# Kernel optimization log

Hardware: AMD Instinct MI355X
Metric: run time of the kernel (lower is better)

Reference implementation:

```python
import jax, jax.numpy as jnp
import numpy as np

NH, HD, MBS = 32, 64, 16   # num_heads, head_dim, mini_batch_size
BASE_LR = 1.0
ROPE_BASE = 10000.0
EPS = 1e-6


def _rotate_half(x):
    x1, x2 = jnp.split(x, 2, axis=-1)
    return jnp.concatenate((-x2, x1), axis=-1)


def _permute_qk(x):
    B, H, L, D = x.shape
    return x.reshape(B, H, L, D // 2, 2).swapaxes(-1, -2).reshape(B, H, L, D)


def _undo_permute_qk(x):
    B, H, L, D = x.shape
    return x.reshape(B, H, L, 2, D // 2).swapaxes(-1, -2).reshape(B, H, L, D)


def _ln_fwd(x, gamma, beta):
    mu = x.mean(-1, keepdims=True)
    var = x.var(-1, keepdims=True)
    return gamma * ((x - mu) / jnp.sqrt(var + EPS)) + beta


def _ln_fused_l2_bwd(x, target, gamma, beta):
    # grad of 0.5*||LN(x) - target||^2 wrt x, fused
    D = x.shape[-1]
    mu = x.mean(-1, keepdims=True)
    std = jnp.sqrt(x.var(-1, keepdims=True) + EPS)
    x_hat = (x - mu) / std
    y = gamma * x_hat + beta
    g = (y - target) * gamma
    return (D * g - g.sum(-1, keepdims=True) - x_hat * (g * x_hat).sum(-1, keepdims=True)) / (D * std)


def setup_inputs() -> dict:
    key = jax.random.key(0)
    ks = jax.random.split(key, 8)
    B, L, C, OUT = 4, 2048, 2048, 768
    s = 0.02
    return {
        "hidden_states": jax.random.normal(ks[0], (B, L, C), jnp.float32),
        "position_ids": jnp.broadcast_to(jnp.arange(L, dtype=jnp.int32)[None], (B, L)),
        "Wq": jax.random.normal(ks[1], (C, C), jnp.float32) * s,
        "Wk": jax.random.normal(ks[2], (C, C), jnp.float32) * s,
        "Wv": jax.random.normal(ks[3], (C, C), jnp.float32) * s,
        "Wo": jax.random.normal(ks[4], (C, OUT), jnp.float32) * s,
        "W1": jax.random.normal(ks[5], (NH, HD, HD), jnp.float32) * s,
        "b1": jnp.zeros((NH, 1, HD), jnp.float32),
        "ttt_lr_weight": jax.random.normal(ks[6], (NH, 1, C), jnp.float32) * s,
        "ttt_lr_bias": jnp.zeros((NH, 1), jnp.float32),
        "learnable_token_idx": jnp.zeros((MBS,), jnp.float32),
        "ttt_norm_weight": jnp.ones((NH, HD), jnp.float32),
        "ttt_norm_bias": jnp.zeros((NH, HD), jnp.float32),
        "post_norm_weight": jnp.ones((C,), jnp.float32),
        "post_norm_bias": jnp.zeros((C,), jnp.float32),
    }


def reference(hidden_states, position_ids, Wq, Wk, Wv, Wo, W1, b1,
              ttt_lr_weight, ttt_lr_bias, learnable_token_idx,
              ttt_norm_weight, ttt_norm_bias, post_norm_weight, post_norm_bias):
    B, L, C = hidden_states.shape
    NM = L // MBS
    # QKV projections -> [B, NH, L, HD]
    XQ = (hidden_states @ Wq).reshape(B, L, NH, HD).transpose(0, 2, 1, 3)
    XK = (hidden_states @ Wk).reshape(B, L, NH, HD).transpose(0, 2, 1, 3)
    XV = (hidden_states @ Wv).reshape(B, L, NH, HD).transpose(0, 2, 1, 3)
    # RoPE on positions modulo the mini-batch size
    pos = (position_ids % MBS).astype(jnp.float32)  # [B, L]
    inv_freq = 1.0 / (ROPE_BASE ** (jnp.arange(0, HD, 2, dtype=jnp.float32) / HD))
    freqs = pos[..., None] * inv_freq               # [B, L, HD/2]
    emb = jnp.concatenate((freqs, freqs), axis=-1)  # [B, L, HD]
    cos = jnp.cos(emb)[:, None]                     # [B, 1, L, HD]
    sin = jnp.sin(emb)[:, None]
    XQ, XK = _permute_qk(XQ), _permute_qk(XK)
    XQ = XQ * cos + _rotate_half(XQ) * sin
    XK = XK * cos + _rotate_half(XK) * sin
    XQ, XK = _undo_permute_qk(XQ), _undo_permute_qk(XK)
    # reshape into mini-batches: [B, NH, NM, K, HD]
    X = hidden_states.reshape(B, NM, MBS, C)
    XQ = XQ.reshape(B, NH, NM, MBS, HD)
    XK = XK.reshape(B, NH, NM, MBS, HD)
    XV = XV.reshape(B, NH, NM, MBS, HD)
    # eta: per-token learnable LR gate
    ttt_lr = jax.nn.sigmoid(
        jnp.einsum('bnkc,hdc->bhnkd', X, ttt_lr_weight)
        + ttt_lr_bias.reshape(1, NH, 1, 1, 1))              # [B,NH,NM,K,1]
    ttt_lr_eta = BASE_LR * ttt_lr.transpose(0, 1, 2, 4, 3) / HD  # [B,NH,NM,1,K]
    token_idx = jnp.clip(1.0 / jnp.arange(1, MBS + 1, dtype=jnp.float32)
                         + learnable_token_idx, 0.0, None)
    token_eta = token_idx.reshape(1, 1, 1, MBS, 1)
    eta = token_eta * ttt_lr_eta                            # [B,NH,NM,K,K]
    # TTT-Linear dual-form mini-batch scan
    ln_w = ttt_norm_weight.reshape(1, NH, 1, HD)
    ln_b = ttt_norm_bias.reshape(1, NH, 1, HD)
    W1_0 = jnp.broadcast_to(W1[None], (B, NH, HD, HD))
    b1_0 = jnp.broadcast_to(b1[None], (B, NH, 1, HD))
    tril = jnp.tril(jnp.ones((MBS, MBS), hidden_states.dtype))

    def step(carry, xs):
        W1_s, b1_s = carry
        xq, xk, xv, eta_m = xs                 # [B,NH,K,HD], eta_m [B,NH,K,K]
        Z1 = xk @ W1_s + b1_s
        target = xv - xk
        grad = _ln_fused_l2_bwd(Z1, target, ln_w, ln_b)
        Attn = tril * (xq @ xk.swapaxes(-1, -2))
        b1_bar = b1_s - (tril * eta_m) @ grad
        Z1_bar = xq @ W1_s - (eta_m * Attn) @ grad + b1_bar
        last_eta = eta_m[:, :, -1, :, None]    # [B,NH,K,1]
        W1_new = W1_s - (last_eta * xk).swapaxes(-1, -2) @ grad
        b1_new = b1_s - jnp.sum(last_eta * grad, axis=-2, keepdims=True)
        out = xq + _ln_fwd(Z1_bar, ln_w, ln_b)
        return (W1_new, b1_new), out

    xs = (XQ.transpose(2, 0, 1, 3, 4), XK.transpose(2, 0, 1, 3, 4),
          XV.transpose(2, 0, 1, 3, 4), eta.transpose(2, 0, 1, 3, 4))
    _, outs = jax.lax.scan(step, (W1_0, b1_0), xs)   # [NM,B,NH,K,HD]
    out = outs.transpose(1, 2, 0, 3, 4).reshape(B, NH, L, HD)
    out = out.transpose(0, 2, 1, 3).reshape(B, L, C)
    # post LayerNorm (eps 1e-6) and output projection
    mu = out.mean(-1, keepdims=True)
    var = out.var(-1, keepdims=True)
    out = (out - mu) / jnp.sqrt(var + EPS) * post_norm_weight + post_norm_bias
    return out @ Wo
```

## Files before the change

### kernel.cpp

```cpp
#include <hip/hip_runtime.h>
#include <cstddef>
#include <cstdint>

#define B_DIM   4
#define L_SEQ   2048
#define C_DIM   2048
#define OUT_DIM 768
#define NHEADS  32
#define HDIM    64
#define MBS_    16
#define NMINI   128
#define EPS_    1e-6f

typedef _Float16 half8 __attribute__((ext_vector_type(8)));
typedef _Float16 half4 __attribute__((ext_vector_type(4)));
typedef float floatx4 __attribute__((ext_vector_type(4)));

__device__ __forceinline__ void glds16(const void* g, void* l) {
    __builtin_amdgcn_global_load_lds(
        (const __attribute__((address_space(1))) uint32_t*)g,
        (__attribute__((address_space(3))) uint32_t*)l, 16, 0, 0);
}

__device__ __forceinline__ void split8(const float4 a, const float4 b,
                                       half8& hi, half8& lo) {
    const float x[8] = {a.x, a.y, a.z, a.w, b.x, b.y, b.z, b.w};
#pragma unroll
    for (int e = 0; e < 8; e++) {
        const _Float16 h = (_Float16)x[e];
        hi[e] = h;
        lo[e] = (_Float16)(x[e] - (float)h);
    }
}

__device__ __forceinline__ void split4(const float4 a, half4& hi, half4& lo) {
    const float x[4] = {a.x, a.y, a.z, a.w};
#pragma unroll
    for (int e = 0; e < 4; e++) {
        const _Float16 h = (_Float16)x[e];
        hi[e] = h;
        lo[e] = (_Float16)(x[e] - (float)h);
    }
}

__device__ __forceinline__ uint32_t pack_hl(float v) {
    const _Float16 h = (_Float16)v;
    const _Float16 l = (_Float16)(v - (float)h);
    union { _Float16 f[2]; uint32_t u; } p;
    p.f[0] = h; p.f[1] = l;
    return p.u;
}

__device__ __forceinline__ half8 pairswap(half8 v) {
    union { half8 h; uint32_t u[4]; } a, b;
    a.h = v;
#pragma unroll
    for (int e = 0; e < 4; e++) b.u[e] = (a.u[e] >> 16) | (a.u[e] << 16);
    return b.h;
}

template<int CTRL>
__device__ __forceinline__ float dpp_add(float v) {
    const int x = __builtin_amdgcn_update_dpp(0, __float_as_int(v), CTRL, 0xF, 0xF, false);
    return v + __int_as_float(x);
}
__device__ __forceinline__ float red16(float v) {
    v = dpp_add<0xB1>(v);
    v = dpp_add<0x4E>(v);
    v = dpp_add<0x124>(v);
    v = dpp_add<0x128>(v);
    return v;
}

__device__ __forceinline__ void bar_lgkm() {
    asm volatile("s_waitcnt lgkmcnt(0)\n\ts_barrier" ::: "memory");
}

__global__ __launch_bounds__(256)
void asplit_kernel(const float* __restrict__ A, _Float16* __restrict__ Ahi,
                   _Float16* __restrict__ Alo)
{
    const size_t idx = ((size_t)blockIdx.x * 256 + threadIdx.x) * 16;
    half8 h0, l0, h1, l1;
    {
        const float4 a = *(const float4*)(A + idx);
        const float4 b = *(const float4*)(A + idx + 4);
        split8(a, b, h0, l0);
    }
    {
        const float4 a = *(const float4*)(A + idx + 8);
        const float4 b = *(const float4*)(A + idx + 12);
        split8(a, b, h1, l1);
    }
    *(half8*)(Ahi + idx)     = h0;
    *(half8*)(Ahi + idx + 8) = h1;
    *(half8*)(Alo + idx)     = l0;
    *(half8*)(Alo + idx + 8) = l1;
}

__global__ __launch_bounds__(512)
void gemm8(const _Float16* __restrict__ Ahi, const _Float16* __restrict__ Alo,
           const _Float16* __restrict__ Bhi, const _Float16* __restrict__ Blo,
           float* __restrict__ Cout, int Ndim, int mode, int doRope)
{
    __shared__ __align__(16) _Float16 sAh[3][8192];
    __shared__ __align__(16) _Float16 sAl[3][8192];
    __shared__ __align__(16) _Float16 sBh[3][4096];
    __shared__ __align__(16) _Float16 sBl[3][4096];
    const int tid = threadIdx.x;
    const int nbx = Ndim >> 7;
    const int nwg = gridDim.x;
    int lin = blockIdx.x;
    lin = (lin & 7) * (nwg >> 3) + (lin >> 3);
    const int m0 = (lin / nbx) * 256;
    const int n0 = (lin % nbx) * 128;
    const int K = 2048;

    size_t gA[2];
    int lA[2];
#pragma unroll
    for (int X = 0; X < 2; X++) {
        const int c = X * 512 + tid;
        const int row = c >> 2, s = c & 3;
        const int ks = s ^ ((row >> 1) & 3);
        gA[X] = (size_t)(m0 + row) * K + ks * 8;
        lA[X] = c * 8;
    }
    size_t gB;
    int lB;
    {
        const int row = tid >> 2, s = tid & 3;
        const int ks = s ^ ((row >> 1) & 3);
        gB = (size_t)(n0 + row) * K + ks * 8;
        lB = tid * 8;
    }

    const int lane = tid & 63, q = lane >> 4, lc = lane & 15;
    const int w = tid >> 6, wm = w >> 1, wn = w & 1;
    int offA[4], offB[4];
#pragma unroll
    for (int i = 0; i < 4; i++) {
        const int rA = wm * 64 + i * 16 + lc;
        offA[i] = rA * 32 + ((q ^ ((rA >> 1) & 3)) << 3);
    }
#pragma unroll
    for (int j = 0; j < 4; j++) {
        const int rB = wn * 64 + j * 16 + lc;
        offB[j] = rB * 32 + ((q ^ ((rB >> 1) & 3)) << 3);
    }

    floatx4 acc[4][4];
#pragma unroll
    for (int i = 0; i < 4; i++)
#pragma unroll
        for (int j = 0; j < 4; j++) acc[i][j] = (floatx4)0.0f;

#define STAGE(T)                                                         \
    {                                                                    \
        const int b_ = (T) % 3;                                          \
        const int ko_ = (T) * 32;                                        \
        glds16(Ahi + gA[0] + ko_, &sAh[b_][lA[0]]);                      \
        glds16(Alo + gA[0] + ko_, &sAl[b_][lA[0]]);                      \
        glds16(Ahi + gA[1] + ko_, &sAh[b_][lA[1]]);                      \
        glds16(Alo + gA[1] + ko_, &sAl[b_][lA[1]]);                      \
        glds16(Bhi + gB + ko_,    &sBh[b_][lB]);                         \
        glds16(Blo + gB + ko_,    &sBl[b_][lB]);                         \
    }

#define FRAGS(B_)                                                        \
    half8 ah[4], al[4], bh[4], bl[4];                                    \
    _Pragma("unroll")                                                    \
    for (int i = 0; i < 4; i++) {                                        \
        ah[i] = *(const half8*)&sAh[B_][offA[i]];                        \
        al[i] = *(const half8*)&sAl[B_][offA[i]];                        \
    }                                                                    \
    _Pragma("unroll")                                                    \
    for (int j = 0; j < 4; j++) {                                        \
        bh[j] = *(const half8*)&sBh[B_][offB[j]];                        \
        bl[j] = *(const half8*)&sBl[B_][offB[j]];                        \
    }

#define MFMAS                                                            \
    __builtin_amdgcn_s_setprio(1);                                       \
    _Pragma("unroll")                                                    \
    for (int i = 0; i < 4; i++)                                          \
        _Pragma("unroll")                                                \
        for (int j = 0; j < 4; j++) {                                    \
            acc[i][j] = __builtin_amdgcn_mfma_f32_16x16x32_f16(ah[i], bh[j], acc[i][j], 0, 0, 0); \
            acc[i][j] = __builtin_amdgcn_mfma_f32_16x16x32_f16(ah[i], bl[j], acc[i][j], 0, 0, 0); \
            acc[i][j] = __builtin_amdgcn_mfma_f32_16x16x32_f16(al[i], bh[j], acc[i][j], 0, 0, 0); \
        }                                                                \
    __builtin_amdgcn_s_setprio(0);

    STAGE(0)
    STAGE(1)
    asm volatile("s_waitcnt vmcnt(6) lgkmcnt(0)\n\ts_barrier" ::: "memory");

    for (int t = 0; t < 62; t++) {
        const int b = t % 3;
        FRAGS(b)
        STAGE(t + 2)
        MFMAS
        asm volatile("s_waitcnt vmcnt(6) lgkmcnt(0)\n\ts_barrier" ::: "memory");
    }
    {
        FRAGS(2)
        MFMAS
        asm volatile("s_waitcnt vmcnt(0) lgkmcnt(0)\n\ts_barrier" ::: "memory");
    }
    {
        FRAGS(0)
        MFMAS
    }
#undef STAGE
#undef FRAGS
#undef MFMAS

    float cs[4][4], sn[4][4];
    if (doRope) {
#pragma unroll
        for (int j = 0; j < 4; j++) {
            const int ii = ((j * 16 + lc) & 63) >> 1;
            const float invf = expf(-(float)ii * 0.28782313662425574f);
#pragma unroll
            for (int r = 0; r < 4; r++) {
                const float ang = (float)(q * 4 + r) * invf;
                sincosf(ang, &sn[j][r], &cs[j][r]);
            }
        }
    }
    const int oddcol = lc & 1;
#pragma unroll
    for (int i = 0; i < 4; i++) {
#pragma unroll
        for (int j = 0; j < 4; j++) {
            floatx4 v = acc[i][j];
            if (doRope) {
#pragma unroll
                for (int r = 0; r < 4; r++) {
                    const float partner = __shfl_xor(v[r], 1);
                    v[r] = v[r] * cs[j][r] + partner * (oddcol ? sn[j][r] : -sn[j][r]);
                }
            }
            const int n = n0 + wn * 64 + j * 16 + lc;
            if (mode == 0) {
                const int h = (n >> 6) & 31, d = n & 63;
#pragma unroll
                for (int r = 0; r < 4; r++) {
                    const int m = m0 + wm * 64 + i * 16 + q * 4 + r;
                    const int b = m >> 11, li = m & 2047;
                    Cout[((size_t)(b * 32 + h) * 2048 + li) * 64 + d] = v[r];
                }
            } else {
#pragma unroll
                for (int r = 0; r < 4; r++) {
                    const int m = m0 + wm * 64 + i * 16 + q * 4 + r;
                    Cout[(size_t)m * OUT_DIM + n] = v[r];
                }
            }
        }
    }
}

__global__ __launch_bounds__(256)
void gemm_f32(const float* __restrict__ A,
              const _Float16* __restrict__ Bhi, const _Float16* __restrict__ Blo,
              float* __restrict__ Cout, int mode, int doRope)
{
    __shared__ __align__(16) float    sA[4096];
    __shared__ __align__(16) _Float16 sBhi[4096];
    __shared__ __align__(16) _Float16 sBlo[4096];
    const int tid = threadIdx.x;
    const int m0 = blockIdx.y * 128, n0 = blockIdx.x * 128;
    const int K = 2048;

    size_t gA[4]; float* lA[4];
#pragma unroll
    for (int I = 0; I < 4; I++) {
        const int c = I * 256 + tid;
        const int row = c >> 3, seg = (c & 7) ^ (row & 7);
        gA[I] = (size_t)(m0 + row) * K + seg * 4;
        lA[I] = &sA[c * 4];
    }
    size_t gB[2]; _Float16 *lBh[2], *lBl[2];
#pragma unroll
    for (int I = 0; I < 2; I++) {
        const int c = I * 256 + tid;
        const int row = c >> 2, seg = (c & 3) ^ ((row >> 1) & 3);
        gB[I] = (size_t)(n0 + row) * K + seg * 8;
        lBh[I] = &sBhi[c * 8];
        lBl[I] = &sBlo[c * 8];
    }

    const int lane = tid & 63, quad = lane >> 4, lc = lane & 15;
    const int wv = tid >> 6, wm = wv & 1, wn = wv >> 1;
    int offA0[4], offA1[4], offB[4];
#pragma unroll
    for (int i = 0; i < 4; i++) {
        const int rA = wm * 64 + i * 16 + lc;
        offA0[i] = (rA * 8 + ((2 * quad)     ^ (rA & 7))) * 4;
        offA1[i] = (rA * 8 + ((2 * quad + 1) ^ (rA & 7))) * 4;
    }
#pragma unroll
    for (int j = 0; j < 4; j++) {
        const int rB = wn * 64 + j * 16 + lc;
        offB[j] = (rB * 4 + (quad ^ ((rB >> 1) & 3))) * 8;
    }

    floatx4 acc[4][4];
#pragma unroll
    for (int i = 0; i < 4; i++)
#pragma unroll
        for (int j = 0; j < 4; j++) acc[i][j] = (floatx4)0.0f;

    for (int k0 = 0; k0 < K; k0 += 32) {
        __syncthreads();
#pragma unroll
        for (int I = 0; I < 4; I++) glds16(A + gA[I] + k0, lA[I]);
#pragma unroll
        for (int I = 0; I < 2; I++) {
            glds16(Bhi + gB[I] + k0, lBh[I]);
            glds16(Blo + gB[I] + k0, lBl[I]);
        }
        __syncthreads();

        half8 ah[4], al[4], bh[4], bl[4];
#pragma unroll
        for (int i = 0; i < 4; i++) {
            const float4 va = *(const float4*)&sA[offA0[i]];
            const float4 vb = *(const float4*)&sA[offA1[i]];
            split8(va, vb, ah[i], al[i]);
        }
#pragma unroll
        for (int j = 0; j < 4; j++) {
            bh[j] = *(const half8*)&sBhi[offB[j]];
            bl[j] = *(const half8*)&sBlo[offB[j]];
        }
#pragma unroll
        for (int i = 0; i < 4; i++)
#pragma unroll
            for (int j = 0; j < 4; j++) {
                acc[i][j] = __builtin_amdgcn_mfma_f32_16x16x32_f16(ah[i], bh[j], acc[i][j], 0, 0, 0);
                acc[i][j] = __builtin_amdgcn_mfma_f32_16x16x32_f16(ah[i], bl[j], acc[i][j], 0, 0, 0);
                acc[i][j] = __builtin_amdgcn_mfma_f32_16x16x32_f16(al[i], bh[j], acc[i][j], 0, 0, 0);
            }
    }

    float cs[4][4], sn[4][4];
    if (doRope) {
#pragma unroll
        for (int j = 0; j < 4; j++) {
            const int ii = ((j * 16 + lc) & 63) >> 1;
            const float invf = expf(-(float)ii * 0.28782313662425574f);
#pragma unroll
            for (int r = 0; r < 4; r++) {
                const float ang = (float)(quad * 4 + r) * invf;
                sincosf(ang, &sn[j][r], &cs[j][r]);
            }
        }
    }
    const int oddcol = lc & 1;
#pragma unroll
    for (int i = 0; i < 4; i++) {
#pragma unroll
        for (int j = 0; j < 4; j++) {
            floatx4 v = acc[i][j];
            if (doRope) {
#pragma unroll
                for (int r = 0; r < 4; r++) {
                    const float partner = __shfl_xor(v[r], 1);
                    v[r] = v[r] * cs[j][r] + partner * (oddcol ? sn[j][r] : -sn[j][r]);
                }
            }
            const int n = n0 + wn * 64 + j * 16 + lc;
            if (mode == 0) {
                const int h = (n >> 6) & 31, d = n & 63;
#pragma unroll
                for (int r = 0; r < 4; r++) {
                    const int m = m0 + wm * 64 + i * 16 + quad * 4 + r;
                    const int b = m >> 11, li = m & 2047;
                    Cout[((size_t)(b * 32 + h) * 2048 + li) * 64 + d] = v[r];
                }
            } else {
#pragma unroll
                for (int r = 0; r < 4; r++) {
                    const int m = m0 + wm * 64 + i * 16 + quad * 4 + r;
                    Cout[(size_t)m * OUT_DIM + n] = v[r];
                }
            }
        }
    }
}

__global__ __launch_bounds__(256)
void wtrans_kernel(const float* __restrict__ W, _Float16* __restrict__ BThi,
                   _Float16* __restrict__ BTlo, int Nw)
{
    __shared__ float tile[32][33];
    const int t = threadIdx.x, tx = t & 31, ty = t >> 5;
    const int n0 = blockIdx.x * 32, k0 = blockIdx.y * 32;
    const int K = 2048;
#pragma unroll
    for (int r = 0; r < 4; r++)
        tile[ty + r * 8][tx] = W[(size_t)(k0 + ty + r * 8) * Nw + n0 + tx];
    __syncthreads();
#pragma unroll
    for (int r = 0; r < 4; r++) {
        const float val = tile[tx][ty + r * 8];
        const _Float16 hh = (_Float16)val;
        const size_t o = (size_t)(n0 + ty + r * 8) * K + k0 + tx;
        BThi[o] = hh;
        BTlo[o] = (_Float16)(val - (float)hh);
    }
}

__global__ __launch_bounds__(256)
void lr_kernel(const float* __restrict__ hidden, const float* __restrict__ wlr,
               const float* __restrict__ lr_bias, float* __restrict__ lrs)
{
    __shared__ float sRow[2048];
    __shared__ float sPart[32][9];
    const int m = blockIdx.x;
    const int t = threadIdx.x;
    const float* row = hidden + (size_t)m * C_DIM;
#pragma unroll
    for (int j = 0; j < 8; j++) sRow[t + j * 256] = row[t + j * 256];
    __syncthreads();
    const int h = t >> 3, p = t & 7;
    const float* w = wlr + (size_t)h * C_DIM;
    float s = 0.0f;
#pragma unroll 8
    for (int k = 0; k < 64; k++) {
        const int c = k * 32 + p * 4;
        const float4 a = *(const float4*)(sRow + c);
        const float4 b = *(const float4*)(w + c);
        s += a.x * b.x + a.y * b.y + a.z * b.z + a.w * b.w;
    }
    sPart[h][p] = s;
    __syncthreads();
    if (t < 32) {
        float v = 0.0f;
#pragma unroll
        for (int p2 = 0; p2 < 8; p2++) v += sPart[t][p2];
        v += lr_bias[t];
        const float sig = 1.0f / (1.0f + expf(-v));
        lrs[((size_t)(m >> 11) * NHEADS + t) * L_SEQ + (m & 2047)] = sig;
    }
}

__global__ __launch_bounds__(256, 1)
void scan_mfma(const float* __restrict__ XQ, const float* __restrict__ XK,
               float* __restrict__ XVo, const float* __restrict__ LRS,
               const float* __restrict__ W1i, const float* __restrict__ b1i,
               const float* __restrict__ lt, const float* __restrict__ lnw,
               const float* __restrict__ lnb)
{
    __shared__ __align__(16) _Float16 sXqH[1024], sXqL[1024];
    __shared__ __align__(16) _Float16 sXkH[1024], sXkL[1024];
    __shared__ __align__(16) float    sTgt[16 * 68];
    __shared__ __align__(16) float    sXq32[2][16 * 68];
    __shared__ __align__(16) _Float16 sW1H[4096], sW1L[4096];
    __shared__ __align__(16) uint32_t sKT[64 * 20];
    __shared__ __align__(16) uint32_t sCf[16 * 20];
    __shared__ __align__(16) float sRedA[16 * 36];
    __shared__ __align__(16) float sRedC[16 * 12];
    __shared__ __align__(16) float sEta[16];
    __shared__ float sB1[64];

    const int bh = blockIdx.x, h = bh & 31;
    const int t = threadIdx.x;
    const int lane = t & 63, q = lane >> 4, lc = lane & 15;
    const int w = t >> 6;
    const int col = w * 16 + lc;
    const int iRow = t >> 4;
    const int m = t & 15;

    if (t < 64) sB1[t] = b1i[h * 64 + t];

    float w1s[4][4];
#pragma unroll
    for (int t4 = 0; t4 < 4; t4++)
#pragma unroll
        for (int r = 0; r < 4; r++) {
            const float v = W1i[h * 4096 + (16 * t4 + lc) * 64 + (16 * w + 4 * q + r)];
            w1s[t4][r] = v;
            const int nn = 16 * w + 4 * q + r, k = 16 * t4 + lc;
            const int off = nn * 64 + ((((k >> 3) ^ (nn & 7)) << 3) | (k & 7));
            const _Float16 hh = (_Float16)v;
            sW1H[off] = hh; sW1L[off] = (_Float16)(v - (float)hh);
        }

    const float gamC = lnw[h * 64 + col], betC = lnb[h * 64 + col];
    const float g2c = gamC * gamC;
    float sumG2 = 0.0f;
#pragma unroll
    for (int d0 = 0; d0 < 16; d0++) {
        const float4 gv = *(const float4*)(lnw + h * 64 + d0 * 4);
        sumG2 += gv.x * gv.x + gv.y * gv.y + gv.z * gv.z + gv.w * gv.w;
    }
    float tokR[4];
#pragma unroll
    for (int r = 0; r < 4; r++)
        tokR[r] = fmaxf(1.0f / (float)(4 * q + r + 1) + lt[4 * q + r], 0.0f);
    const float tok15 = fmaxf(1.0f / 16.0f + lt[15], 0.0f);

    __syncthreads();

    const size_t base = (size_t)bh * L_SEQ * HDIM;
    const float* xq_g = XQ + base;
    const float* xk_g = XK + base;
    float* xv_g = XVo + base;
    const float* lr_g = LRS + (size_t)bh * L_SEQ;

    float4 cq = *(const float4*)(xq_g + t * 4);
    float4 ck = *(const float4*)(xk_g + t * 4);
    float4 cv = *(const float4*)(xv_g + t * 4);
    float clr = lr_g[m];

    const int rw = 16 * w + lc;
    const int stOff = iRow * 64 + ((((m >> 1) ^ (iRow & 7)) << 3) | ((m & 1) << 2));
    const int gkm = (m ^ (m >> 2)) & 3;
    const int ktWb = 4 * (w ^ gkm) + q;

    for (int n = 0; n < NMINI; n++) {
        const int buf = n & 1;
        {
            half4 hq, lq, hk, lk;
            split4(cq, hq, lq);
            split4(ck, hk, lk);
            *(half4*)&sXqH[stOff] = hq;
            *(half4*)&sXqL[stOff] = lq;
            *(half4*)&sXkH[stOff] = hk;
            *(half4*)&sXkL[stOff] = lk;
            const float4 tg = make_float4(cv.x - ck.x, cv.y - ck.y,
                                          cv.z - ck.z, cv.w - ck.w);
            *(float4*)&sTgt[iRow * 68 + m * 4] = tg;
            *(float4*)&sXq32[buf][iRow * 68 + m * 4] = cq;
            const float kvv[4] = {ck.x, ck.y, ck.z, ck.w};
#pragma unroll
            for (int i2 = 0; i2 < 4; i2++)
                sKT[(4 * m + i2) * 20 + ktWb] = pack_hl(kvv[i2]);
        }
        if (t < 16) sEta[t] = clr * (1.0f / 64.0f);
        const int np = (n + 1) & (NMINI - 1);
        const float4 nq = *(const float4*)(xq_g + np * 1024 + t * 4);
        const float4 nk = *(const float4*)(xk_g + np * 1024 + t * 4);
        const float4 nv = *(const float4*)(xv_g + np * 1024 + t * 4);
        const float nlr = lr_g[np * 16 + m];
        bar_lgkm();

        const float b1c = sB1[col];
        const float4 ev = *(const float4*)&sEta[4 * q];
        const float evv[4] = {ev.x, ev.y, ev.z, ev.w};

        half8 qh[2], ql[2], kh[2], kl[2], wh[2], wl[2];
#pragma unroll
        for (int f = 0; f < 2; f++) {
            const int cx = ((4 * f + q) ^ (lc & 7)) << 3;
            qh[f] = *(const half8*)&sXqH[lc * 64 + cx];
            ql[f] = *(const half8*)&sXqL[lc * 64 + cx];
            kh[f] = *(const half8*)&sXkH[lc * 64 + cx];
            kl[f] = *(const half8*)&sXkL[lc * 64 + cx];
            const int cw = ((4 * f + q) ^ (rw & 7)) << 3;
            wh[f] = *(const half8*)&sW1H[rw * 64 + cw];
            wl[f] = *(const half8*)&sW1L[rw * 64 + cw];
        }

        floatx4 z1a = (floatx4)0.0f, zba = (floatx4)0.0f, at = (floatx4)0.0f;
#pragma unroll
        for (int f = 0; f < 2; f++) {
            z1a = __builtin_amdgcn_mfma_f32_16x16x32_f16(kh[f], wh[f], z1a, 0, 0, 0);
            z1a = __builtin_amdgcn_mfma_f32_16x16x32_f16(kh[f], wl[f], z1a, 0, 0, 0);
            z1a = __builtin_amdgcn_mfma_f32_16x16x32_f16(kl[f], wh[f], z1a, 0, 0, 0);
            zba = __builtin_amdgcn_mfma_f32_16x16x32_f16(qh[f], wh[f], zba, 0, 0, 0);
            zba = __builtin_amdgcn_mfma_f32_16x16x32_f16(qh[f], wl[f], zba, 0, 0, 0);
            zba = __builtin_amdgcn_mfma_f32_16x16x32_f16(ql[f], wh[f], zba, 0, 0, 0);
        }
        if (w == 0) {
            const float etaLC = sEta[lc];
#pragma unroll
            for (int f = 0; f < 2; f++) {
                at = __builtin_amdgcn_mfma_f32_16x16x32_f16(qh[f], kh[f], at, 0, 0, 0);
                at = __builtin_amdgcn_mfma_f32_16x16x32_f16(qh[f], kl[f], at, 0, 0, 0);
                at = __builtin_amdgcn_mfma_f32_16x16x32_f16(ql[f], kh[f], at, 0, 0, 0);
            }
#pragma unroll
            for (int r = 0; r < 4; r++) {
                const int i = 4 * q + r;
                const float cfv = (lc <= i) ? -tokR[r] * etaLC * (at[r] + 1.0f) : 0.0f;
                sCf[i * 20 + 4 * ((lc >> 2) ^ q) + (lc & 3)] = pack_hl(cfv);
            }
        }

        float z[4], cE[4];
        float sz[4], szz[4], sgz[4], sgzz[4], sc[4], scz[4];
#pragma unroll
        for (int r = 0; r < 4; r++) {
            const int row = 4 * q + r;
            z[r] = z1a[r] + b1c;
            const float tgt = sTgt[row * 68 + col];
            cE[r] = gamC * (betC - tgt);
            const float zz = z[r] * z[r];
            sz[r]   = red16(z[r]);
            szz[r]  = red16(zz);
            sgz[r]  = red16(g2c * z[r]);
            sgzz[r] = red16(g2c * zz);
            sc[r]   = red16(cE[r]);
            scz[r]  = red16(cE[r] * z[r]);
        }
        if (lc == 0) {
#pragma unroll
            for (int r = 0; r < 4; r++) {
                const int rb = (4 * q + r) * 36;
                sRedA[rb + 0  + w] = sz[r];
                sRedA[rb + 4  + w] = szz[r];
                sRedA[rb + 8  + w] = sgz[r];
                sRedA[rb + 12 + w] = sgzz[r];
                sRedA[rb + 16 + w] = sc[r];
                sRedA[rb + 20 + w] = scz[r];
            }
        }
        bar_lgkm();

        half8 ktp[4];
#pragma unroll
        for (int t4 = 0; t4 < 4; t4++) {
            const int gkr = ((lc >> 2) ^ t4) & 3;
            ktp[t4] = *(const half8*)&sKT[(16 * t4 + lc) * 20 + 4 * (q ^ gkr)];
        }
        const half8 cfp = *(const half8*)&sCf[lc * 20 + 4 * (q ^ (lc >> 2))];

        float gr[4];
#pragma unroll
        for (int r = 0; r < 4; r++) {
            const int rb = (4 * q + r) * 36;
            const float4 a0 = *(const float4*)&sRedA[rb + 0];
            const float4 a1 = *(const float4*)&sRedA[rb + 4];
            const float4 a2 = *(const float4*)&sRedA[rb + 8];
            const float4 a3 = *(const float4*)&sRedA[rb + 12];
            const float4 a4 = *(const float4*)&sRedA[rb + 16];
            const float4 a5 = *(const float4*)&sRedA[rb + 20];
            const float Sz   = a0.x + a0.y + a0.z + a0.w;
            const float Szz  = a1.x + a1.y + a1.z + a1.w;
            const float Sgz  = a2.x + a2.y + a2.z + a2.w;
            const float Sgzz = a3.x + a3.y + a3.z + a3.w;
            const float Sc   = a4.x + a4.y + a4.z + a4.w;
            const float Scz  = a5.x + a5.y + a5.z + a5.w;
            const float mu  = Sz * (1.0f / 64.0f);
            const float ex2 = Szz * (1.0f / 64.0f);
            const float rs  = rsqrtf(ex2 - mu * mu + EPS_);
            const float G1 = rs * (Sgz - mu * sumG2) + Sc;
            const float G2 = rs * rs * (Sgzz - 2.0f * mu * Sgz + mu * mu * sumG2)
                           + rs * (Scz - mu * Sc);
            const float xh = (z[r] - mu) * rs;
            const float g  = g2c * xh + cE[r];
            gr[r] = (64.0f * g - G1 - xh * G2) * rs * (1.0f / 64.0f);
        }

        half8 gf, gfl;
#pragma unroll
        for (int r = 0; r < 4; r++) {
            const _Float16 h0 = (_Float16)gr[r];
            gf[2 * r]     = h0;
            gf[2 * r + 1] = (_Float16)(gr[r] - (float)h0);
            const float gl = gr[r] * (tok15 * evv[r]);
            const _Float16 h1 = (_Float16)gl;
            gfl[2 * r]     = h1;
            gfl[2 * r + 1] = (_Float16)(gl - (float)h1);
        }
        const half8 gfs  = pairswap(gf);
        const half8 gfls = pairswap(gfl);

        zba = __builtin_amdgcn_mfma_f32_16x16x32_f16(cfp, gf,  zba, 0, 0, 0);
        zba = __builtin_amdgcn_mfma_f32_16x16x32_f16(cfp, gfs, zba, 0, 0, 0);
#pragma unroll
        for (int t4 = 0; t4 < 4; t4++) {
            floatx4 up = (floatx4)0.0f;
            up = __builtin_amdgcn_mfma_f32_16x16x32_f16(gfl,  ktp[t4], up, 0, 0, 0);
            up = __builtin_amdgcn_mfma_f32_16x16x32_f16(gfls, ktp[t4], up, 0, 0, 0);
#pragma unroll
            for (int r = 0; r < 4; r++) w1s[t4][r] -= up[r];
        }

        float z2[4], p1[4], p2[4];
#pragma unroll
        for (int r = 0; r < 4; r++) {
            z2[r] = zba[r] + b1c;
            p1[r] = red16(z2[r]);
            p2[r] = red16(z2[r] * z2[r]);
        }
        if (lc == 0)
#pragma unroll
            for (int r = 0; r < 4; r++) {
                const int rb = (4 * q + r) * 12;
                sRedC[rb + w]     = p1[r];
                sRedC[rb + 4 + w] = p2[r];
            }

        {
            float p = gr[0] * evv[0] + gr[1] * evv[1] + gr[2] * evv[2] + gr[3] * evv[3];
            p += __shfl_xor(p, 16);
            p += __shfl_xor(p, 32);
            if (q == 0) sB1[col] -= tok15 * p;
        }
#pragma unroll
        for (int t4 = 0; t4 < 4; t4++)
#pragma unroll
            for (int r = 0; r < 4; r++) {
                const int nn = 16 * w + 4 * q + r, k = 16 * t4 + lc;
                const int off = nn * 64 + ((((k >> 3) ^ (nn & 7)) << 3) | (k & 7));
                const float v = w1s[t4][r];
                const _Float16 hh = (_Float16)v;
                sW1H[off] = hh; sW1L[off] = (_Float16)(v - (float)hh);
            }
        bar_lgkm();

#pragma unroll
        for (int r = 0; r < 4; r++) {
            const int row = 4 * q + r;
            const float4 a = *(const float4*)&sRedC[row * 12];
            const float4 b = *(const float4*)&sRedC[row * 12 + 4];
            const float mu  = (a.x + a.y + a.z + a.w) * (1.0f / 64.0f);
            const float ex2 = (b.x + b.y + b.z + b.w) * (1.0f / 64.0f);
            const float rs  = rsqrtf(ex2 - mu * mu + EPS_);
            const float xqv = sXq32[buf][row * 68 + col];
            xv_g[n * 1024 + row * 64 + col] = xqv + gamC * ((z2[r] - mu) * rs) + betC;
        }
        cq = nq; ck = nk; cv = nv; clr = nlr;
    }
}

__global__ __launch_bounds__(256)
void postln_kernel(const float* __restrict__ Ob, const float* __restrict__ pnw,
                   const float* __restrict__ pnb, _Float16* __restrict__ XNhi,
                   _Float16* __restrict__ XNlo)
{
    const int m = blockIdx.x;
    const int b = m >> 11, l = m & 2047;
    const int t = threadIdx.x;
    float v[8];
    float s1 = 0.0f, s2 = 0.0f;
    const int c0 = t * 8;
    const int hh = c0 >> 6, d0 = c0 & 63;
    const float* bas = Ob + (size_t)b * NHEADS * L_SEQ * HDIM + (size_t)l * HDIM
                     + (size_t)hh * (L_SEQ * HDIM) + d0;
    {
        const float4 va = *(const float4*)(bas);
        const float4 vb = *(const float4*)(bas + 4);
        v[0] = va.x; v[1] = va.y; v[2] = va.z; v[3] = va.w;
        v[4] = vb.x; v[5] = vb.y; v[6] = vb.z; v[7] = vb.w;
    }
#pragma unroll
    for (int j = 0; j < 8; j++) { s1 += v[j]; s2 += v[j] * v[j]; }
#pragma unroll
    for (int o = 1; o < 64; o <<= 1) { s1 += __shfl_xor(s1, o); s2 += __shfl_xor(s2, o); }
    __shared__ float r1[4], r2[4];
    const int w = t >> 6;
    if ((t & 63) == 0) { r1[w] = s1; r2[w] = s2; }
    __syncthreads();
    s1 = r1[0] + r1[1] + r1[2] + r1[3];
    s2 = r2[0] + r2[1] + r2[2] + r2[3];
    const float mu = s1 * (1.0f / 2048.0f);
    const float var = s2 * (1.0f / 2048.0f) - mu * mu;
    const float rstd = rsqrtf(var + EPS_);
    half8 oh, ol;
#pragma unroll
    for (int j = 0; j < 8; j++) {
        const float y = (v[j] - mu) * rstd * pnw[c0 + j] + pnb[c0 + j];
        const _Float16 hy = (_Float16)y;
        oh[j] = hy;
        ol[j] = (_Float16)(y - (float)hy);
    }
    *(half8*)(XNhi + (size_t)m * C_DIM + c0) = oh;
    *(half8*)(XNlo + (size_t)m * C_DIM + c0) = ol;
}

extern "C" void kernel_launch(void* const* d_in, const int* in_sizes, int n_in,
                              void* d_out, int out_size, void* d_ws, size_t ws_size,
                              hipStream_t stream)
{
    (void)in_sizes; (void)n_in; (void)out_size;
    const float* hidden  = (const float*)d_in[0];
    const float* Wq      = (const float*)d_in[2];
    const float* Wk      = (const float*)d_in[3];
    const float* Wv      = (const float*)d_in[4];
    const float* Wo      = (const float*)d_in[5];
    const float* W1      = (const float*)d_in[6];
    const float* b1      = (const float*)d_in[7];
    const float* wlr     = (const float*)d_in[8];
    const float* lr_bias = (const float*)d_in[9];
    const float* lt      = (const float*)d_in[10];
    const float* lnw     = (const float*)d_in[11];
    const float* lnb     = (const float*)d_in[12];
    const float* pnw     = (const float*)d_in[13];
    const float* pnb     = (const float*)d_in[14];

    const size_t TEN = (size_t)B_DIM * NHEADS * L_SEQ * HDIM;
    float* XQ  = (float*)d_ws;
    float* XK  = XQ + TEN;
    float* XVo = XK + TEN;
    float* LRS = XVo + TEN;
    _Float16* Ahi = (_Float16*)(LRS + 262144);
    _Float16* Alo = Ahi + TEN;
    const size_t needBytes = (3 * TEN + 262144) * 4 + TEN * 4;
    const int useAsplit = (ws_size >= needBytes) ? 1 : 0;
    const dim3 blk(256);

    _Float16* BThi = (_Float16*)d_out;
    _Float16* BTlo = BThi + (size_t)C_DIM * C_DIM;

    lr_kernel<<<dim3(B_DIM * L_SEQ), blk, 0, stream>>>(hidden, wlr, lr_bias, LRS);
    if (useAsplit)
        asplit_kernel<<<dim3(4096), blk, 0, stream>>>(hidden, Ahi, Alo);

    const float* Wmats[3] = {Wq, Wk, Wv};
    float* outs[3] = {XQ, XK, XVo};
    for (int p = 0; p < 3; p++) {
        wtrans_kernel<<<dim3(64, 64), blk, 0, stream>>>(Wmats[p], BThi, BTlo, C_DIM);
        if (useAsplit)
            gemm8<<<dim3(512), dim3(512), 0, stream>>>(Ahi, Alo, BThi, BTlo,
                                                       outs[p], C_DIM,
                                                       0, (p < 2) ? 1 : 0);
        else
            gemm_f32<<<dim3(16, 64), blk, 0, stream>>>(hidden, BThi, BTlo,
                                                       outs[p], 0, (p < 2) ? 1 : 0);
    }
    scan_mfma<<<dim3(B_DIM * NHEADS), blk, 0, stream>>>(XQ, XK, XVo, LRS,
                                                        W1, b1, lt, lnw, lnb);
    _Float16* XNhi = (_Float16*)XQ;
    _Float16* XNlo = XNhi + TEN;
    _Float16* WThi = (_Float16*)XK;
    _Float16* WTlo = WThi + (size_t)OUT_DIM * C_DIM;
    postln_kernel<<<dim3(B_DIM * L_SEQ), blk, 0, stream>>>(XVo, pnw, pnb,
                                                           XNhi, XNlo);
    wtrans_kernel<<<dim3(24, 64), blk, 0, stream>>>(Wo, WThi, WTlo, OUT_DIM);
    gemm8<<<dim3(192), dim3(512), 0, stream>>>(XNhi, XNlo, WThi, WTlo,
                                               (float*)d_out, OUT_DIM, 1, 0);
}
```

Measured before the change: 1.402 ms.

## Interleave GEMM prefetch with MFMAs and defer scan output LN to next iteration

In the split-fp16 GEMM main loop, fragment loads and global-to-LDS prefetch are now interleaved with the MFMA groups per row-tile instead of issued all up front. In the scan kernel, the final LayerNorm and store of each mini-batch output move into the next iteration after its first barrier, which removes one barrier per step. The key-transpose buffer is double-buffered to make that safe, and the next-chunk loads are hoisted earlier. Accumulator chains in the Z1/Zbar/attention MFMAs are split in two for more ILP. These changes add registers and extra LDS and rely on the sRedC and sXq32 contents surviving across the barrier.

Measured after the change: 1.423 ms. No clear change (+1.5%).

```diff
diff --git a/kernel.cpp b/kernel.cpp
--- a/kernel.cpp
+++ b/kernel.cpp
@@ -155,7 +155,7 @@
 #pragma unroll
         for (int j = 0; j < 4; j++) acc[i][j] = (floatx4)0.0f;
 
-#define STAGE(T)                                                         \
+#define STAGE_ALL(T)                                                     \
     {                                                                    \
         const int b_ = (T) % 3;                                          \
         const int ko_ = (T) * 32;                                        \
@@ -167,54 +167,85 @@
         glds16(Blo + gB + ko_,    &sBl[b_][lB]);                         \
     }
 
-#define FRAGS(B_)                                                        \
-    half8 ah[4], al[4], bh[4], bl[4];                                    \
-    _Pragma("unroll")                                                    \
-    for (int i = 0; i < 4; i++) {                                        \
-        ah[i] = *(const half8*)&sAh[B_][offA[i]];                        \
-        al[i] = *(const half8*)&sAl[B_][offA[i]];                        \
-    }                                                                    \
+#define MFMA_I(i)                                                        \
+    __builtin_amdgcn_s_setprio(1);                                       \
     _Pragma("unroll")                                                    \
     for (int j = 0; j < 4; j++) {                                        \
-        bh[j] = *(const half8*)&sBh[B_][offB[j]];                        \
-        bl[j] = *(const half8*)&sBl[B_][offB[j]];                        \
-    }
-
-#define MFMAS                                                            \
-    __builtin_amdgcn_s_setprio(1);                                       \
-    _Pragma("unroll")                                                    \
-    for (int i = 0; i < 4; i++)                                          \
-        _Pragma("unroll")                                                \
-        for (int j = 0; j < 4; j++) {                                    \
-            acc[i][j] = __builtin_amdgcn_mfma_f32_16x16x32_f16(ah[i], bh[j], acc[i][j], 0, 0, 0); \
-            acc[i][j] = __builtin_amdgcn_mfma_f32_16x16x32_f16(ah[i], bl[j], acc[i][j], 0, 0, 0); \
-            acc[i][j] = __builtin_amdgcn_mfma_f32_16x16x32_f16(al[i], bh[j], acc[i][j], 0, 0, 0); \
-        }                                                                \
+        acc[i][j] = __builtin_amdgcn_mfma_f32_16x16x32_f16(ah[i], bh[j], acc[i][j], 0, 0, 0); \
+        acc[i][j] = __builtin_amdgcn_mfma_f32_16x16x32_f16(ah[i], bl[j], acc[i][j], 0, 0, 0); \
+        acc[i][j] = __builtin_amdgcn_mfma_f32_16x16x32_f16(al[i], bh[j], acc[i][j], 0, 0, 0); \
+    }                                                                    \
     __builtin_amdgcn_s_setprio(0);
 
-    STAGE(0)
-    STAGE(1)
+    STAGE_ALL(0)
+    STAGE_ALL(1)
     asm volatile("s_waitcnt vmcnt(6) lgkmcnt(0)\n\ts_barrier" ::: "memory");
 
     for (int t = 0; t < 62; t++) {
         const int b = t % 3;
-        FRAGS(b)
-        STAGE(t + 2)
-        MFMAS
+        const int b2 = (t + 2) % 3;
+        const int ko2 = (t + 2) * 32;
+        half8 ah[4], al[4], bh[4], bl[4];
+#pragma unroll
+        for (int j = 0; j < 4; j++) {
+            bh[j] = *(const half8*)&sBh[b][offB[j]];
+            bl[j] = *(const half8*)&sBl[b][offB[j]];
+        }
+        ah[0] = *(const half8*)&sAh[b][offA[0]];
+        al[0] = *(const half8*)&sAl[b][offA[0]];
+        glds16(Ahi + gA[0] + ko2, &sAh[b2][lA[0]]);
+        glds16(Alo + gA[0] + ko2, &sAl[b2][lA[0]]);
+        bar_lgkm();
+        MFMA_I(0)
+        ah[1] = *(const half8*)&sAh[b][offA[1]];
+        al[1] = *(const half8*)&sAl[b][offA[1]];
+        glds16(Ahi + gA[1] + ko2, &sAh[b2][lA[1]]);
+        glds16(Alo + gA[1] + ko2, &sAl[b2][lA[1]]);
+        bar_lgkm();
+        MFMA_I(1)
+        ah[2] = *(const half8*)&sAh[b][offA[2]];
+        al[2] = *(const half8*)&sAl[b][offA[2]];
+        glds16(Bhi + gB + ko2, &sBh[b2][lB]);
+        glds16(Blo + gB + ko2, &sBl[b2][lB]);
+        bar_lgkm();
+        MFMA_I(2)
+        ah[3] = *(const half8*)&sAh[b][offA[3]];
+        al[3] = *(const half8*)&sAl[b][offA[3]];
         asm volatile("s_waitcnt vmcnt(6) lgkmcnt(0)\n\ts_barrier" ::: "memory");
+        MFMA_I(3)
     }
     {
-        FRAGS(2)
-        MFMAS
-        asm volatile("s_waitcnt vmcnt(0) lgkmcnt(0)\n\ts_barrier" ::: "memory");
+        half8 ah[4], al[4], bh[4], bl[4];
+#pragma unroll
+        for (int j = 0; j < 4; j++) {
+            bh[j] = *(const half8*)&sBh[2][offB[j]];
+            bl[j] = *(const half8*)&sBl[2][offB[j]];
+        }
+#pragma unroll
+        for (int i = 0; i < 4; i++) {
+            ah[i] = *(const half8*)&sAh[2][offA[i]];
+            al[i] = *(const half8*)&sAl[2][offA[i]];
+        }
+        asm volatile("s_waitcnt vmcnt(0) lgkmcnt(0)" ::: "memory");
+        MFMA_I(0) MFMA_I(1) MFMA_I(2) MFMA_I(3)
+        __syncthreads();
     }
     {
-        FRAGS(0)
-        MFMAS
-    }
-#undef STAGE
-#undef FRAGS
-#undef MFMAS
+        half8 ah[4], al[4], bh[4], bl[4];
+#pragma unroll
+        for (int j = 0; j < 4; j++) {
+            bh[j] = *(const half8*)&sBh[0][offB[j]];
+            bl[j] = *(const half8*)&sBl[0][offB[j]];
+        }
+#pragma unroll
+        for (int i = 0; i < 4; i++) {
+            ah[i] = *(const half8*)&sAh[0][offA[i]];
+            al[i] = *(const half8*)&sAl[0][offA[i]];
+        }
+        MFMA_I(0) MFMA_I(1) MFMA_I(2) MFMA_I(3)
+    }
+#undef STAGE_ALL
+#undef MFMA_I
 
     float cs[4][4], sn[4][4];
     if (doRope) {
@@ -460,7 +491,7 @@
     __shared__ __align__(16) float    sTgt[16 * 68];
     __shared__ __align__(16) float    sXq32[2][16 * 68];
     __shared__ __align__(16) _Float16 sW1H[4096], sW1L[4096];
-    __shared__ __align__(16) uint32_t sKT[64 * 20];
+    __shared__ __align__(16) uint32_t sKT[2][64 * 20];
     __shared__ __align__(16) uint32_t sCf[16 * 20];
     __shared__ __align__(16) float sRedA[16 * 36];
     __shared__ __align__(16) float sRedC[16 * 12];
@@ -522,8 +553,15 @@
     const int gkm = (m ^ (m >> 2)) & 3;
     const int ktWb = 4 * (w ^ gkm) + q;
 
+    float z2p[4] = {0.0f, 0.0f, 0.0f, 0.0f};
+
     for (int n = 0; n < NMINI; n++) {
         const int buf = n & 1;
+        const int np = (n + 1) & (NMINI - 1);
+        const float4 nq = *(const float4*)(xq_g + np * 1024 + t * 4);
+        const float4 nk = *(const float4*)(xk_g + np * 1024 + t * 4);
+        const float4 nv = *(const float4*)(xv_g + np * 1024 + t * 4);
+        const float nlr = lr_g[np * 16 + m];
         {
             half4 hq, lq, hk, lk;
             split4(cq, hq, lq);
@@ -539,15 +577,26 @@
             const float kvv[4] = {ck.x, ck.y, ck.z, ck.w};
 #pragma unroll
             for (int i2 = 0; i2 < 4; i2++)
-                sKT[(4 * m + i2) * 20 + ktWb] = pack_hl(kvv[i2]);
+                sKT[buf][(4 * m + i2) * 20 + ktWb] = pack_hl(kvv[i2]);
         }
         if (t < 16) sEta[t] = clr * (1.0f / 64.0f);
-        const int np = (n + 1) & (NMINI - 1);
-        const float4 nq = *(const float4*)(xq_g + np * 1024 + t * 4);
-        const float4 nk = *(const float4*)(xk_g + np * 1024 + t * 4);
-        const float4 nv = *(const float4*)(xv_g + np * 1024 + t * 4);
-        const float nlr = lr_g[np * 16 + m];
         bar_lgkm();
+
+        if (n) {
+            const int pb = buf ^ 1;
+#pragma unroll
+            for (int r = 0; r < 4; r++) {
+                const int row = 4 * q + r;
+                const float4 a = *(const float4*)&sRedC[row * 12];
+                const float4 b = *(const float4*)&sRedC[row * 12 + 4];
+                const float mu  = (a.x + a.y + a.z + a.w) * (1.0f / 64.0f);
+                const float ex2 = (b.x + b.y + b.z + b.w) * (1.0f / 64.0f);
+                const float rs  = rsqrtf(ex2 - mu * mu + EPS_);
+                const float xqv = sXq32[pb][row * 68 + col];
+                xv_g[(n - 1) * 1024 + row * 64 + col] =
+                    xqv + gamC * ((z2p[r] - mu) * rs) + betC;
+            }
+        }
 
         const float b1c = sB1[col];
         const float4 ev = *(const float4*)&sEta[4 * q];
@@ -566,28 +615,34 @@
             wl[f] = *(const half8*)&sW1L[rw * 64 + cw];
         }
 
-        floatx4 z1a = (floatx4)0.0f, zba = (floatx4)0.0f, at = (floatx4)0.0f;
-#pragma unroll
-        for (int f = 0; f < 2; f++) {
-            z1a = __builtin_amdgcn_mfma_f32_16x16x32_f16(kh[f], wh[f], z1a, 0, 0, 0);
-            z1a = __builtin_amdgcn_mfma_f32_16x16x32_f16(kh[f], wl[f], z1a, 0, 0, 0);
-            z1a = __builtin_amdgcn_mfma_f32_16x16x32_f16(kl[f], wh[f], z1a, 0, 0, 0);
-            zba = __builtin_amdgcn_mfma_f32_16x16x32_f16(qh[f], wh[f], zba, 0, 0, 0);
-            zba = __builtin_amdgcn_mfma_f32_16x16x32_f16(qh[f], wl[f], zba, 0, 0, 0);
-            zba = __builtin_amdgcn_mfma_f32_16x16x32_f16(ql[f], wh[f], zba, 0, 0, 0);
-        }
+        floatx4 z1a = (floatx4)0.0f, z1b = (floatx4)0.0f;
+        floatx4 zb0 = (floatx4)0.0f, zb1 = (floatx4)0.0f;
+        z1a = __builtin_amdgcn_mfma_f32_16x16x32_f16(kh[0], wh[0], z1a, 0, 0, 0);
+        z1a = __builtin_amdgcn_mfma_f32_16x16x32_f16(kh[0], wl[0], z1a, 0, 0, 0);
+        z1a = __builtin_amdgcn_mfma_f32_16x16x32_f16(kl[0], wh[0], z1a, 0, 0, 0);
+        z1b = __builtin_amdgcn_mfma_f32_16x16x32_f16(kh[1], wh[1], z1b, 0, 0, 0);
+        z1b = __builtin_amdgcn_mfma_f32_16x16x32_f16(kh[1], wl[1], z1b, 0, 0, 0);
+        z1b = __builtin_amdgcn_mfma_f32_16x16x32_f16(kl[1], wh[1], z1b, 0, 0, 0);
+        zb0 = __builtin_amdgcn_mfma_f32_16x16x32_f16(qh[0], wh[0], zb0, 0, 0, 0);
+        zb0 = __builtin_amdgcn_mfma_f32_16x16x32_f16(qh[0], wl[0], zb0, 0, 0, 0);
+        zb0 = __builtin_amdgcn_mfma_f32_16x16x32_f16(ql[0], wh[0], zb0, 0, 0, 0);
+        zb1 = __builtin_amdgcn_mfma_f32_16x16x32_f16(qh[1], wh[1], zb1, 0, 0, 0);
+        zb1 = __builtin_amdgcn_mfma_f32_16x16x32_f16(qh[1], wl[1], zb1, 0, 0, 0);
+        zb1 = __builtin_amdgcn_mfma_f32_16x16x32_f16(ql[1], wh[1], zb1, 0, 0, 0);
         if (w == 0) {
             const float etaLC = sEta[lc];
-#pragma unroll
-            for (int f = 0; f < 2; f++) {
-                at = __builtin_amdgcn_mfma_f32_16x16x32_f16(qh[f], kh[f], at, 0, 0, 0);
-                at = __builtin_amdgcn_mfma_f32_16x16x32_f16(qh[f], kl[f], at, 0, 0, 0);
-                at = __builtin_amdgcn_mfma_f32_16x16x32_f16(ql[f], kh[f], at, 0, 0, 0);
-            }
+            floatx4 at0 = (floatx4)0.0f, at1 = (floatx4)0.0f;
+            at0 = __builtin_amdgcn_mfma_f32_16x16x32_f16(qh[0], kh[0], at0, 0, 0, 0);
+            at0 = __builtin_amdgcn_mfma_f32_16x16x32_f16(qh[0], kl[0], at0, 0, 0, 0);
+            at0 = __builtin_amdgcn_mfma_f32_16x16x32_f16(ql[0], kh[0], at0, 0, 0, 0);
+            at1 = __builtin_amdgcn_mfma_f32_16x16x32_f16(qh[1], kh[1], at1, 0, 0, 0);
+            at1 = __builtin_amdgcn_mfma_f32_16x16x32_f16(qh[1], kl[1], at1, 0, 0, 0);
+            at1 = __builtin_amdgcn_mfma_f32_16x16x32_f16(ql[1], kh[1], at1, 0, 0, 0);
 #pragma unroll
             for (int r = 0; r < 4; r++) {
                 const int i = 4 * q + r;
-                const float cfv = (lc <= i) ? -tokR[r] * etaLC * (at[r] + 1.0f) : 0.0f;
+                const float atv = at0[r] + at1[r];
+                const float cfv = (lc <= i) ? -tokR[r] * etaLC * (atv + 1.0f) : 0.0f;
                 sCf[i * 20 + 4 * ((lc >> 2) ^ q) + (lc & 3)] = pack_hl(cfv);
             }
         }
@@ -597,7 +652,7 @@
 #pragma unroll
         for (int r = 0; r < 4; r++) {
             const int row = 4 * q + r;
-            z[r] = z1a[r] + b1c;
+            z[r] = z1a[r] + z1b[r] + b1c;
             const float tgt = sTgt[row * 68 + col];
             cE[r] = gamC * (betC - tgt);
             const float zz = z[r] * z[r];
@@ -626,7 +681,7 @@
 #pragma unroll
         for (int t4 = 0; t4 < 4; t4++) {
             const int gkr = ((lc >> 2) ^ t4) & 3;
-            ktp[t4] = *(const half8*)&sKT[(16 * t4 + lc) * 20 + 4 * (q ^ gkr)];
+            ktp[t4] = *(const half8*)&sKT[buf][(16 * t4 + lc) * 20 + 4 * (q ^ gkr)];
         }
         const half8 cfp = *(const half8*)&sCf[lc * 20 + 4 * (q ^ (lc >> 2))];
 
@@ -671,6 +726,9 @@
         const half8 gfs  = pairswap(gf);
         const half8 gfls = pairswap(gfl);
 
+        floatx4 zba;
+#pragma unroll
+        for (int r = 0; r < 4; r++) zba[r] = zb0[r] + zb1[r];
         zba = __builtin_amdgcn_mfma_f32_16x16x32_f16(cfp, gf,  zba, 0, 0, 0);
         zba = __builtin_amdgcn_mfma_f32_16x16x32_f16(cfp, gfs, zba, 0, 0, 0);
 #pragma unroll
@@ -713,20 +771,24 @@
                 const _Float16 hh = (_Float16)v;
                 sW1H[off] = hh; sW1L[off] = (_Float16)(v - (float)hh);
             }
-        bar_lgkm();
-
-#pragma unroll
-        for (int r = 0; r < 4; r++) {
-            const int row = 4 * q + r;
-            const float4 a = *(const float4*)&sRedC[row * 12];
-            const float4 b = *(const float4*)&sRedC[row * 12 + 4];
-            const float mu  = (a.x + a.y + a.z + a.w) * (1.0f / 64.0f);
-            const float ex2 = (b.x + b.y + b.z + b.w) * (1.0f / 64.0f);
-            const float rs  = rsqrtf(ex2 - mu * mu + EPS_);
-            const float xqv = sXq32[buf][row * 68 + col];
-            xv_g[n * 1024 + row * 64 + col] = xqv + gamC * ((z2[r] - mu) * rs) + betC;
-        }
+
+#pragma unroll
+        for (int r = 0; r < 4; r++) z2p[r] = z2[r];
         cq = nq; ck = nk; cv = nv; clr = nlr;
+    }
+
+    bar_lgkm();
+#pragma unroll
+    for (int r = 0; r < 4; r++) {
+        const int row = 4 * q + r;
+        const float4 a = *(const float4*)&sRedC[row * 12];
+        const float4 b = *(const float4*)&sRedC[row * 12 + 4];
+        const float mu  = (a.x + a.y + a.z + a.w) * (1.0f / 64.0f);
+        const float ex2 = (b.x + b.y + b.z + b.w) * (1.0f / 64.0f);
+        const float rs  = rsqrtf(ex2 - mu * mu + EPS_);
+        const float xqv = sXq32[1][row * 68 + col];
+        xv_g[(NMINI - 1) * 1024 + row * 64 + col] =
+            xqv + gamC * ((z2p[r] - mu) * rs) + betC;
     }
 }
 
```
